# Kernel optimization log

Hardware: AMD Instinct MI355X
Metric: run time of the kernel (lower is better)

The kernel has to match this reference:

```python
import jax, jax.numpy as jnp
import numpy as np


def setup_inputs() -> dict:
    key = jax.random.key(0)
    k1, k2, k3 = jax.random.split(key, 3)
    b, n, h, d = 2, 2048, 16, 64
    q = jax.random.normal(k1, (b, n, h, d), dtype=jnp.float32)
    k = jax.random.normal(k2, (b, n, h, d), dtype=jnp.float32)
    v = jax.random.normal(k3, (b, n, h, d), dtype=jnp.float32)
    return {"q": q, "k": k, "v": v, "is_causal": 1}


def reference(q, k, v, is_causal):
    # q, k, v: [b, n, h, d] -> attention computed in [b, h, n, d] layout
    b, n, h, d = q.shape
    scale = 1.0 / jnp.sqrt(jnp.asarray(d, dtype=q.dtype))
    # scores: [b, h, n_q, n_k]
    scores = jnp.einsum("bqhd,bkhd->bhqk", q, k) * scale
    if is_causal:
        causal_mask = jnp.triu(jnp.ones((n, n), dtype=bool), k=1)  # True above diag
        scores = jnp.where(causal_mask[None, None], -jnp.inf, scores)
    attn = jax.nn.softmax(scores, axis=-1)
    out = jnp.einsum("bhqk,bkhd->bqhd", attn, v)  # back to [b, n, h, d]
    return out
```

## Files before the change

kernel.cpp:

```cpp
#include <hip/hip_runtime.h>
#include <hip/hip_bf16.h>

namespace {

constexpr int Nn = 2048;
constexpr int Hh = 16;
constexpr int Dd = 64;
constexpr int ROWSTR = Hh * Dd;
constexpr int KVB = 64;
constexpr int NTILES = Nn / KVB;
constexpr size_t IMG_TILE = 16384;
constexpr size_t WS_NEED = (size_t)32 * NTILES * IMG_TILE;

typedef __bf16 bf16x8 __attribute__((ext_vector_type(8)));
typedef __bf16 bf16x4 __attribute__((ext_vector_type(4)));
typedef float  f32x16 __attribute__((ext_vector_type(16)));

constexpr float MSHIFT = 16.0f;

__device__ __forceinline__ void gload_lds16(const char* g, char* l) {
  __builtin_amdgcn_global_load_lds(
      (const __attribute__((address_space(1))) void*)g,
      (__attribute__((address_space(3))) void*)l, 16, 0, 0);
}
__device__ __forceinline__ void drain_vmcnt0() {
  asm volatile("s_waitcnt vmcnt(0)" ::: "memory");
}

__global__ __launch_bounds__(256, 2) void prep_kernel(
    const float* __restrict__ Kg, const float* __restrict__ Vg,
    char* __restrict__ ws) {
  const int bid = blockIdx.x;
  const int bh  = bid & 31;
  const int T   = bid >> 5;
  const int tid = threadIdx.x;
  const int b = bh >> 4, h = bh & 15;
  const size_t base = ((size_t)b * Nn * Hh + h) * Dd;
  const float* kp = Kg + base;
  const float* vp = Vg + base;
  char* img = ws + (size_t)(bh * NTILES + T) * IMG_TILE;

  {
    const int row = tid >> 2;
    const int seg = tid & 3;
    const float* kr = kp + (size_t)(T * 64 + row) * ROWSTR + seg * 16;
    float4 f0 = ((const float4*)kr)[0];
    float4 f1 = ((const float4*)kr)[1];
    float4 f2 = ((const float4*)kr)[2];
    float4 f3 = ((const float4*)kr)[3];
    const int half = row >> 5, l31r = row & 31;
    char* slotp = img + (half * 4 + seg) * 1024;
    bf16x8 w0 = { (__bf16)f0.x, (__bf16)f0.y, (__bf16)f0.z, (__bf16)f0.w,
                  (__bf16)f1.x, (__bf16)f1.y, (__bf16)f1.z, (__bf16)f1.w };
    bf16x8 w1 = { (__bf16)f2.x, (__bf16)f2.y, (__bf16)f2.z, (__bf16)f2.w,
                  (__bf16)f3.x, (__bf16)f3.y, (__bf16)f3.z, (__bf16)f3.w };
    *(bf16x8*)(slotp + l31r * 16) = w0;
    *(bf16x8*)(slotp + (l31r + 32) * 16) = w1;
  }
  char* imgV = img + 8192;
#pragma unroll
  for (int e2 = 0; e2 < 2; ++e2) {
    const int e = e2 * 256 + tid;
    const int slotV = e >> 6, lane = e & 63;
    const int kc = slotV >> 1, df = slotV & 1;
    const int l31e = lane & 31, g2e = lane >> 5;
    const int d = 32 * df + l31e;
    const size_t kv0 = (size_t)(T * 64 + 16 * kc + 4 * g2e);
    const float* vb = vp + d;
    bf16x8 w;
#pragma unroll
    for (int i2 = 0; i2 < 4; ++i2) w[i2]     = (__bf16)vb[(kv0 + i2) * ROWSTR];
#pragma unroll
    for (int i2 = 0; i2 < 4; ++i2) w[4 + i2] = (__bf16)vb[(kv0 + 8 + i2) * ROWSTR];
    *(bf16x8*)(imgV + slotV * 1024 + lane * 16) = w;
  }
}

__global__ __launch_bounds__(256, 2) void fattn_kernel(
    const float* __restrict__ Qg, const char* __restrict__ ws,
    const int* __restrict__ flag, float* __restrict__ Og) {
  __shared__ __align__(16) char smem[2][2][16384];

  const int tid  = threadIdx.x;
  const int lane = tid & 63;
  const int wv   = tid >> 6;
  const int l31  = lane & 31;
  const int g2   = lane >> 5;

  const int bid  = blockIdx.x;
  const int r    = bid >> 1;
  const int side = bid & 1;
  const int bh   = ((r & 7) << 2) | ((r >> 3) & 3);
  const int j    = r >> 5;
  const int Tq   = side ? j : (15 - j);
  const int b    = bh >> 4;
  const int h    = bh & 15;
  const int causal = flag[0];

  const size_t base = ((size_t)b * Nn * Hh + h) * Dd;
  const float* qp = Qg + base;
  const char*  img = ws + (size_t)bh * NTILES * IMG_TILE;
  float*       op = Og + base;

  const float SCALE = 0.125f * 1.44269504088896340736f;

  bf16x8 vone;
#pragma unroll
  for (int e = 0; e < 8; ++e) vone[e] = (__bf16)1.0f;

  const int qs  = Tq * 128 + wv * 32;
  const int NI  = causal ? (Tq + 1) : (NTILES / 2);
  const int TLw = causal ? (2 * Tq + (wv >> 1)) : (NTILES - 1);

  bf16x8 qf[4];
#pragma unroll
  for (int dc = 0; dc < 4; ++dc) {
    const float* qrow = qp + (size_t)(qs + l31) * ROWSTR + dc * 16 + g2 * 8;
    float4 a = *(const float4*)qrow;
    float4 c = *(const float4*)(qrow + 4);
    qf[dc][0] = (__bf16)(a.x * SCALE); qf[dc][1] = (__bf16)(a.y * SCALE);
    qf[dc][2] = (__bf16)(a.z * SCALE); qf[dc][3] = (__bf16)(a.w * SCALE);
    qf[dc][4] = (__bf16)(c.x * SCALE); qf[dc][5] = (__bf16)(c.y * SCALE);
    qf[dc][6] = (__bf16)(c.z * SCALE); qf[dc][7] = (__bf16)(c.w * SCALE);
  }

  f32x16 acc0 = {};
  f32x16 acc1 = {};
  f32x16 accl = {};

#pragma unroll
  for (int it = 0; it < 8; ++it)
    gload_lds16(img + (it * 256 + tid) * 16,
                &smem[0][0][0] + (it * 256 + tid) * 16);
  __builtin_amdgcn_sched_barrier(0);

  for (int i = 0; i < NI; ++i) {
    drain_vmcnt0();
    __syncthreads();
    if (i + 1 < NI) {
      const char* src = img + (size_t)(2 * i + 2) * IMG_TILE;
      char* dst = &smem[(i + 1) & 1][0][0];
#pragma unroll
      for (int it = 0; it < 8; ++it)
        gload_lds16(src + (it * 256 + tid) * 16, dst + (it * 256 + tid) * 16);
      __builtin_amdgcn_sched_barrier(0);
    }

#pragma unroll
    for (int halfT = 0; halfT < 2; ++halfT) {
      const int tt = 2 * i + halfT;
      if (tt <= TLw) {
        const char* kb = &smem[i & 1][halfT][0];
        const char* vb = kb + 8192;

        f32x16 s0, s1;
#pragma unroll
        for (int rr = 0; rr < 16; ++rr) { s0[rr] = -MSHIFT; s1[rr] = -MSHIFT; }
        __builtin_amdgcn_s_setprio(1);
#pragma unroll
        for (int dc = 0; dc < 4; ++dc) {
          bf16x8 kf0 = *(const bf16x8*)(kb + (dc)     * 1024 + lane * 16);
          bf16x8 kf1 = *(const bf16x8*)(kb + (4 + dc) * 1024 + lane * 16);
          s0 = __builtin_amdgcn_mfma_f32_32x32x16_bf16(kf0, qf[dc], s0, 0, 0, 0);
          s1 = __builtin_amdgcn_mfma_f32_32x32x16_bf16(kf1, qf[dc], s1, 0, 0, 0);
        }
        __builtin_amdgcn_s_setprio(0);

        if (causal && tt == TLw) {
          const int kvb = tt * KVB;
          const int qrow = qs + l31;
#pragma unroll
          for (int rr = 0; rr < 16; ++rr) {
            int rm = (rr & 3) + ((rr >> 2) << 3) + (g2 << 2);
            if (kvb + rm > qrow)      s0[rr] = -INFINITY;
            if (kvb + 32 + rm > qrow) s1[rr] = -INFINITY;
          }
        }

#pragma unroll
        for (int rr = 0; rr < 16; ++rr) {
          s0[rr] = __builtin_amdgcn_exp2f(s0[rr]);
          s1[rr] = __builtin_amdgcn_exp2f(s1[rr]);
        }

        bf16x8 pa[4];
#pragma unroll
        for (int kc = 0; kc < 4; ++kc) {
          const f32x16& sv = (kc < 2) ? s0 : s1;
          const int rbase = (kc & 1) * 8;
#pragma unroll
          for (int jj = 0; jj < 8; ++jj) pa[kc][jj] = (__bf16)sv[rbase + jj];
        }

        __builtin_amdgcn_s_setprio(1);
#pragma unroll
        for (int kc = 0; kc < 4; ++kc) {
          bf16x8 vf0 = *(const bf16x8*)(vb + (kc * 2)     * 1024 + lane * 16);
          bf16x8 vf1 = *(const bf16x8*)(vb + (kc * 2 + 1) * 1024 + lane * 16);
          acc0 = __builtin_amdgcn_mfma_f32_32x32x16_bf16(pa[kc], vf0, acc0, 0, 0, 0);
          acc1 = __builtin_amdgcn_mfma_f32_32x32x16_bf16(pa[kc], vf1, acc1, 0, 0, 0);
          accl = __builtin_amdgcn_mfma_f32_32x32x16_bf16(pa[kc], vone, accl, 0, 0, 0);
        }
        __builtin_amdgcn_s_setprio(0);
      }
    }
  }

#pragma unroll
  for (int rr = 0; rr < 16; ++rr) {
    const int rm = (rr & 3) + ((rr >> 2) << 3) + (g2 << 2);
    const float li = 1.0f / accl[rr];
    const size_t row = (size_t)(qs + rm) * ROWSTR;
    op[row + l31]      = acc0[rr] * li;
    op[row + 32 + l31] = acc1[rr] * li;
  }
}

__device__ __forceinline__ int swzK(int row, int colByte) {
  return (row * 128 + colByte) ^ ((row & 7) << 4);
}
__device__ __forceinline__ int swzV(int row, int colByte) {
  return (row * 128 + colByte) ^ (((row & 7) << 4) | (((row >> 3) & 1) << 3));
}
struct SR { float4 k[4]; float v[16]; };
__device__ __forceinline__ void fb_issue(const float* kp, const float* vp,
                                         int kv0, int tid, SR& s) {
#pragma unroll
  for (int it = 0; it < 4; ++it) {
    int idx = it * 256 + tid;
    int kvr = idx >> 4, c4 = idx & 15;
    s.k[it] = *(const float4*)(kp + (size_t)(kv0 + kvr) * ROWSTR + c4 * 4);
  }
#pragma unroll
  for (int it = 0; it < 4; ++it) {
    int idx = it * 256 + tid;
    int d8 = idx & 63, kv4 = idx >> 6;
#pragma unroll
    for (int i2 = 0; i2 < 4; ++i2)
      s.v[it * 4 + i2] = vp[(size_t)(kv0 + kv4 * 4 + i2) * ROWSTR + d8];
  }
}
__device__ __forceinline__ void fb_write(char* kb, char* vb, int tid, const SR& s) {
#pragma unroll
  for (int it = 0; it < 4; ++it) {
    int idx = it * 256 + tid;
    int kvr = idx >> 4, c4 = idx & 15;
    bf16x4 w = { (__bf16)s.k[it].x, (__bf16)s.k[it].y,
                 (__bf16)s.k[it].z, (__bf16)s.k[it].w };
    *(bf16x4*)(kb + swzK(kvr, c4 * 8)) = w;
  }
#pragma unroll
  for (int it = 0; it < 4; ++it) {
    int idx = it * 256 + tid;
    int d8 = idx & 63, kv4 = idx >> 6;
    bf16x4 w = { (__bf16)s.v[it * 4 + 0], (__bf16)s.v[it * 4 + 1],
                 (__bf16)s.v[it * 4 + 2], (__bf16)s.v[it * 4 + 3] };
    *(bf16x4*)(vb + swzV(d8, kv4 * 8)) = w;
  }
}
__global__ __launch_bounds__(256, 2) void fattn_fb(
    const float* __restrict__ Qg, const float* __restrict__ Kg,
    const float* __restrict__ Vg, const int* __restrict__ flag,
    float* __restrict__ Og) {
  __shared__ char smem[16384];
  const int tid  = threadIdx.x;
  const int lane = tid & 63;
  const int wv   = tid >> 6;
  const int l31  = lane & 31;
  const int g2   = lane >> 5;
  const int bid = blockIdx.x;
  const int pidx = bid >> 1;
  const int side = bid & 1;
  const int bh  = ((pidx & 7) << 2) | (pidx >> 6);
  const int ti  = (pidx >> 3) & 7;
  const int b   = bh >> 4;
  const int h   = bh & 15;
  const int causal = flag[0];
  const int Tq  = side ? ti : (15 - ti);
  const size_t base = ((size_t)b * Nn * Hh + h) * Dd;
  const float* qp = Qg + base;
  const float* kp = Kg + base;
  const float* vp = Vg + base;
  float*       op = Og + base;
  const float SCALE = 0.125f * 1.44269504088896340736f;
  const int qs = Tq * 128 + wv * 32;
  const int Tblock = causal ? (2 * Tq + 2) : NTILES;
  const int Twave  = causal ? ((qs + 31) / KVB + 1) : NTILES;
  bf16x8 qf[4];
#pragma unroll
  for (int dc = 0; dc < 4; ++dc) {
    const float* qrow = qp + (size_t)(qs + l31) * ROWSTR + dc * 16 + g2 * 8;
    float4 a = *(const float4*)qrow;
    float4 c = *(const float4*)(qrow + 4);
    qf[dc][0] = (__bf16)(a.x * SCALE); qf[dc][1] = (__bf16)(a.y * SCALE);
    qf[dc][2] = (__bf16)(a.z * SCALE); qf[dc][3] = (__bf16)(a.w * SCALE);
    qf[dc][4] = (__bf16)(c.x * SCALE); qf[dc][5] = (__bf16)(c.y * SCALE);
    qf[dc][6] = (__bf16)(c.z * SCALE); qf[dc][7] = (__bf16)(c.w * SCALE);
  }
  f32x16 acc0 = {}, acc1 = {};
  float m_run = -INFINITY, l_run = 0.0f;
  SR st;
  fb_issue(kp, vp, 0, tid, st);
  fb_write(smem, smem + 8192, tid, st);
  for (int t = 0; t < Tblock; ++t) {
    __syncthreads();
    const bool pf = (t + 1 < Tblock);
    if (pf) fb_issue(kp, vp, (t + 1) * KVB, tid, st);
    if (t < Twave) {
      const char* kb = smem;
      const char* vb = smem + 8192;
      f32x16 s0 = {}, s1 = {};
#pragma unroll
      for (int dc = 0; dc < 4; ++dc) {
        bf16x8 kf0 = *(const bf16x8*)(kb + swzK(l31,      32 * dc + 16 * g2));
        bf16x8 kf1 = *(const bf16x8*)(kb + swzK(32 + l31, 32 * dc + 16 * g2));
        s0 = __builtin_amdgcn_mfma_f32_32x32x16_bf16(kf0, qf[dc], s0, 0, 0, 0);
        s1 = __builtin_amdgcn_mfma_f32_32x32x16_bf16(kf1, qf[dc], s1, 0, 0, 0);
      }
      if (causal && t == Twave - 1) {
        const int kvb = t * KVB;
        const int qrow = qs + l31;
#pragma unroll
        for (int rr = 0; rr < 16; ++rr) {
          int rm = (rr & 3) + ((rr >> 2) << 3) + (g2 << 2);
          if (kvb + rm > qrow)      s0[rr] = -INFINITY;
          if (kvb + 32 + rm > qrow) s1[rr] = -INFINITY;
        }
      }
      float p8[8];
#pragma unroll
      for (int e = 0; e < 8; ++e)
        p8[e] = fmaxf(fmaxf(s0[e], s0[e + 8]), fmaxf(s1[e], s1[e + 8]));
      float mt = fmaxf(fmaxf(fmaxf(p8[0], p8[1]), fmaxf(p8[2], p8[3])),
                       fmaxf(fmaxf(p8[4], p8[5]), fmaxf(p8[6], p8[7])));
      mt = fmaxf(mt, __shfl_xor(mt, 32));
      const float mnew = fmaxf(m_run, mt);
#pragma unroll
      for (int rr = 0; rr < 16; ++rr) {
        s0[rr] = __builtin_amdgcn_exp2f(s0[rr] - mnew);
        s1[rr] = __builtin_amdgcn_exp2f(s1[rr] - mnew);
      }
      float q8[8];
#pragma unroll
      for (int e = 0; e < 8; ++e)
        q8[e] = (s0[e] + s0[e + 8]) + (s1[e] + s1[e + 8]);
      float rs = ((q8[0] + q8[1]) + (q8[2] + q8[3])) +
                 ((q8[4] + q8[5]) + (q8[6] + q8[7]));
      rs += __shfl_xor(rs, 32);
      if (__all(mt <= m_run)) {
        l_run += rs;
      } else {
        const float alpha = __builtin_amdgcn_exp2f(m_run - mnew);
#pragma unroll
        for (int rr = 0; rr < 16; ++rr) {
          float at = __shfl(alpha, (rr & 3) + ((rr >> 2) << 3) + (g2 << 2));
          acc0[rr] *= at;
          acc1[rr] *= at;
        }
        l_run = l_run * alpha + rs;
        m_run = mnew;
      }
      bf16x8 pa[4];
#pragma unroll
      for (int kc = 0; kc < 4; ++kc) {
        const f32x16& sv = (kc < 2) ? s0 : s1;
        const int rbase = (kc & 1) * 8;
#pragma unroll
        for (int jj = 0; jj < 8; ++jj) pa[kc][jj] = (__bf16)sv[rbase + jj];
      }
#pragma unroll
      for (int kc = 0; kc < 4; ++kc) {
        const int cb = 32 * kc + 8 * g2;
#pragma unroll
        for (int df = 0; df < 2; ++df) {
          const int row = 32 * df + l31;
          bf16x4 v0 = *(const bf16x4*)(vb + swzV(row, cb));
          bf16x4 v1 = *(const bf16x4*)(vb + swzV(row, cb + 16));
          bf16x8 vf = __builtin_shufflevector(v0, v1, 0, 1, 2, 3, 4, 5, 6, 7);
          if (df == 0)
            acc0 = __builtin_amdgcn_mfma_f32_32x32x16_bf16(pa[kc], vf, acc0, 0, 0, 0);
          else
            acc1 = __builtin_amdgcn_mfma_f32_32x32x16_bf16(pa[kc], vf, acc1, 0, 0, 0);
        }
      }
    }
    __syncthreads();
    if (pf) fb_write(smem, smem + 8192, tid, st);
  }
  const float linv = 1.0f / l_run;
#pragma unroll
  for (int rr = 0; rr < 16; ++rr) {
    const int rm = (rr & 3) + ((rr >> 2) << 3) + (g2 << 2);
    const float li = __shfl(linv, rm);
    const size_t row = (size_t)(qs + rm) * ROWSTR;
    op[row + l31]      = acc0[rr] * li;
    op[row + 32 + l31] = acc1[rr] * li;
  }
}

}

extern "C" void kernel_launch(void* const* d_in, const int* in_sizes, int n_in,
                              void* d_out, int out_size, void* d_ws, size_t ws_size,
                              hipStream_t stream) {
  (void)in_sizes; (void)n_in; (void)out_size;
  const float* q = (const float*)d_in[0];
  const float* k = (const float*)d_in[1];
  const float* v = (const float*)d_in[2];
  const int* flag = (const int*)d_in[3];
  float* out = (float*)d_out;
  if (ws_size >= WS_NEED) {
    char* ws = (char*)d_ws;
    prep_kernel<<<dim3(1024), dim3(256), 0, stream>>>(k, v, ws);
    fattn_kernel<<<dim3(512), dim3(256), 0, stream>>>(q, ws, flag, out);
  } else {
    fattn_fb<<<dim3(512), dim3(256), 0, stream>>>(q, k, v, flag, out);
  }
}
```

Before: 46.18 us.

## Use 512-thread blocks with 256-row Q tiles, two passes, triple-buffered KV prefetch

Restructures the attention kernel into 256 blocks of 8 waves, each covering a 256-row query tile, with two passes per block that pair a long and a short causal tile for balance. KV tiles are triple-buffered in LDS with a two-ahead prefetch and a partial vmcnt wait, replacing the double buffer with a full drain. This aims to hide global-to-LDS latency and share each KV load across more waves, at the cost of 96KB of LDS per block, which may limit residency to one block per CU, and only 256 blocks launched.

```diff
diff --git a/kernel.cpp b/kernel.cpp
--- a/kernel.cpp
+++ b/kernel.cpp
@@ -22,9 +22,6 @@
   __builtin_amdgcn_global_load_lds(
       (const __attribute__((address_space(1))) void*)g,
       (__attribute__((address_space(3))) void*)l, 16, 0, 0);
-}
-__device__ __forceinline__ void drain_vmcnt0() {
-  asm volatile("s_waitcnt vmcnt(0)" ::: "memory");
 }
 
 __global__ __launch_bounds__(256, 2) void prep_kernel(
@@ -76,10 +73,10 @@
   }
 }
 
-__global__ __launch_bounds__(256, 2) void fattn_kernel(
+__global__ __launch_bounds__(512, 2) void fattn_kernel(
     const float* __restrict__ Qg, const char* __restrict__ ws,
     const int* __restrict__ flag, float* __restrict__ Og) {
-  __shared__ __align__(16) char smem[2][2][16384];
+  __shared__ __align__(16) char smem[3][32768];
 
   const int tid  = threadIdx.x;
   const int lane = tid & 63;
@@ -87,14 +84,11 @@
   const int l31  = lane & 31;
   const int g2   = lane >> 5;
 
-  const int bid  = blockIdx.x;
-  const int r    = bid >> 1;
-  const int side = bid & 1;
-  const int bh   = ((r & 7) << 2) | ((r >> 3) & 3);
-  const int j    = r >> 5;
-  const int Tq   = side ? j : (15 - j);
-  const int b    = bh >> 4;
-  const int h    = bh & 15;
+  const int bid = blockIdx.x;
+  const int bh  = ((bid & 7) << 2) | ((bid >> 3) & 3);
+  const int jp  = bid >> 5;
+  const int b   = bh >> 4;
+  const int h   = bh & 15;
   const int causal = flag[0];
 
   const size_t base = ((size_t)b * Nn * Hh + h) * Dd;
@@ -108,111 +102,129 @@
 #pragma unroll
   for (int e = 0; e < 8; ++e) vone[e] = (__bf16)1.0f;
 
-  const int qs  = Tq * 128 + wv * 32;
-  const int NI  = causal ? (Tq + 1) : (NTILES / 2);
-  const int TLw = causal ? (2 * Tq + (wv >> 1)) : (NTILES - 1);
-
-  bf16x8 qf[4];
-#pragma unroll
-  for (int dc = 0; dc < 4; ++dc) {
-    const float* qrow = qp + (size_t)(qs + l31) * ROWSTR + dc * 16 + g2 * 8;
-    float4 a = *(const float4*)qrow;
-    float4 c = *(const float4*)(qrow + 4);
-    qf[dc][0] = (__bf16)(a.x * SCALE); qf[dc][1] = (__bf16)(a.y * SCALE);
-    qf[dc][2] = (__bf16)(a.z * SCALE); qf[dc][3] = (__bf16)(a.w * SCALE);
-    qf[dc][4] = (__bf16)(c.x * SCALE); qf[dc][5] = (__bf16)(c.y * SCALE);
-    qf[dc][6] = (__bf16)(c.z * SCALE); qf[dc][7] = (__bf16)(c.w * SCALE);
-  }
-
-  f32x16 acc0 = {};
-  f32x16 acc1 = {};
-  f32x16 accl = {};
-
-#pragma unroll
-  for (int it = 0; it < 8; ++it)
-    gload_lds16(img + (it * 256 + tid) * 16,
-                &smem[0][0][0] + (it * 256 + tid) * 16);
-  __builtin_amdgcn_sched_barrier(0);
-
-  for (int i = 0; i < NI; ++i) {
-    drain_vmcnt0();
+  for (int pass = 0; pass < 2; ++pass) {
+    const int T256 = pass ? jp : (7 - jp);
+    const int qs   = T256 * 256 + wv * 32;
+    const int NI   = causal ? (2 * T256 + 2) : (NTILES / 2);
+    const int TLw  = causal ? (4 * T256 + (wv >> 1)) : (NTILES - 1);
+
     __syncthreads();
-    if (i + 1 < NI) {
-      const char* src = img + (size_t)(2 * i + 2) * IMG_TILE;
-      char* dst = &smem[(i + 1) & 1][0][0];
-#pragma unroll
-      for (int it = 0; it < 8; ++it)
-        gload_lds16(src + (it * 256 + tid) * 16, dst + (it * 256 + tid) * 16);
+
+    bf16x8 qf[4];
+#pragma unroll
+    for (int dc = 0; dc < 4; ++dc) {
+      const float* qrow = qp + (size_t)(qs + l31) * ROWSTR + dc * 16 + g2 * 8;
+      float4 a = *(const float4*)qrow;
+      float4 c = *(const float4*)(qrow + 4);
+      qf[dc][0] = (__bf16)(a.x * SCALE); qf[dc][1] = (__bf16)(a.y * SCALE);
+      qf[dc][2] = (__bf16)(a.z * SCALE); qf[dc][3] = (__bf16)(a.w * SCALE);
+      qf[dc][4] = (__bf16)(c.x * SCALE); qf[dc][5] = (__bf16)(c.y * SCALE);
+      qf[dc][6] = (__bf16)(c.z * SCALE); qf[dc][7] = (__bf16)(c.w * SCALE);
+    }
+
+    f32x16 acc0 = {};
+    f32x16 acc1 = {};
+    f32x16 accl = {};
+
+#pragma unroll
+    for (int it = 0; it < 4; ++it)
+      gload_lds16(img + (it * 512 + tid) * 16,
+                  &smem[0][0] + (it * 512 + tid) * 16);
+    if (NI > 1) {
+#pragma unroll
+      for (int it = 0; it < 4; ++it)
+        gload_lds16(img + 2 * IMG_TILE + (it * 512 + tid) * 16,
+                    &smem[1][0] + (it * 512 + tid) * 16);
+    }
+    __builtin_amdgcn_sched_barrier(0);
+
+    for (int i = 0; i < NI; ++i) {
+      if (i + 1 < NI) {
+        asm volatile("s_waitcnt vmcnt(4)" ::: "memory");
+      } else {
+        asm volatile("s_waitcnt vmcnt(0)" ::: "memory");
+      }
       __builtin_amdgcn_sched_barrier(0);
+      __syncthreads();
+
+      if (i + 2 < NI) {
+        const char* src = img + (size_t)(2 * i + 4) * IMG_TILE;
+        char* dst = &smem[(i + 2) % 3][0];
+#pragma unroll
+        for (int it = 0; it < 4; ++it)
+          gload_lds16(src + (it * 512 + tid) * 16, dst + (it * 512 + tid) * 16);
+        __builtin_amdgcn_sched_barrier(0);
+      }
+
+      const char* pb = &smem[i % 3][0];
+#pragma unroll
+      for (int halfT = 0; halfT < 2; ++halfT) {
+        const int tt = 2 * i + halfT;
+        if (tt <= TLw) {
+          const char* kb = pb + halfT * 16384;
+          const char* vb = kb + 8192;
+
+          f32x16 s0, s1;
+#pragma unroll
+          for (int rr = 0; rr < 16; ++rr) { s0[rr] = -MSHIFT; s1[rr] = -MSHIFT; }
+          __builtin_amdgcn_s_setprio(1);
+#pragma unroll
+          for (int dc = 0; dc < 4; ++dc) {
+            bf16x8 kf0 = *(const bf16x8*)(kb + (dc)     * 1024 + lane * 16);
+            bf16x8 kf1 = *(const bf16x8*)(kb + (4 + dc) * 1024 + lane * 16);
+            s0 = __builtin_amdgcn_mfma_f32_32x32x16_bf16(kf0, qf[dc], s0, 0, 0, 0);
+            s1 = __builtin_amdgcn_mfma_f32_32x32x16_bf16(kf1, qf[dc], s1, 0, 0, 0);
+          }
+          __builtin_amdgcn_s_setprio(0);
+
+          if (causal && tt == TLw) {
+            const int kvb = tt * KVB;
+            const int qrow = qs + l31;
+#pragma unroll
+            for (int rr = 0; rr < 16; ++rr) {
+              int rm = (rr & 3) + ((rr >> 2) << 3) + (g2 << 2);
+              if (kvb + rm > qrow)      s0[rr] = -INFINITY;
+              if (kvb + 32 + rm > qrow) s1[rr] = -INFINITY;
+            }
+          }
+
+#pragma unroll
+          for (int rr = 0; rr < 16; ++rr) {
+            s0[rr] = __builtin_amdgcn_exp2f(s0[rr]);
+            s1[rr] = __builtin_amdgcn_exp2f(s1[rr]);
+          }
+
+          bf16x8 pa[4];
+#pragma unroll
+          for (int kc = 0; kc < 4; ++kc) {
+            const f32x16& sv = (kc < 2) ? s0 : s1;
+            const int rbase = (kc & 1) * 8;
+#pragma unroll
+            for (int jj = 0; jj < 8; ++jj) pa[kc][jj] = (__bf16)sv[rbase + jj];
+          }
+
+          __builtin_amdgcn_s_setprio(1);
+#pragma unroll
+          for (int kc = 0; kc < 4; ++kc) {
+            bf16x8 vf0 = *(const bf16x8*)(vb + (kc * 2)     * 1024 + lane * 16);
+            bf16x8 vf1 = *(const bf16x8*)(vb + (kc * 2 + 1) * 1024 + lane * 16);
+            acc0 = __builtin_amdgcn_mfma_f32_32x32x16_bf16(pa[kc], vf0, acc0, 0, 0, 0);
+            acc1 = __builtin_amdgcn_mfma_f32_32x32x16_bf16(pa[kc], vf1, acc1, 0, 0, 0);
+            accl = __builtin_amdgcn_mfma_f32_32x32x16_bf16(pa[kc], vone, accl, 0, 0, 0);
+          }
+          __builtin_amdgcn_s_setprio(0);
+        }
+      }
     }
 
 #pragma unroll
-    for (int halfT = 0; halfT < 2; ++halfT) {
-      const int tt = 2 * i + halfT;
-      if (tt <= TLw) {
-        const char* kb = &smem[i & 1][halfT][0];
-        const char* vb = kb + 8192;
-
-        f32x16 s0, s1;
-#pragma unroll
-        for (int rr = 0; rr < 16; ++rr) { s0[rr] = -MSHIFT; s1[rr] = -MSHIFT; }
-        __builtin_amdgcn_s_setprio(1);
-#pragma unroll
-        for (int dc = 0; dc < 4; ++dc) {
-          bf16x8 kf0 = *(const bf16x8*)(kb + (dc)     * 1024 + lane * 16);
-          bf16x8 kf1 = *(const bf16x8*)(kb + (4 + dc) * 1024 + lane * 16);
-          s0 = __builtin_amdgcn_mfma_f32_32x32x16_bf16(kf0, qf[dc], s0, 0, 0, 0);
-          s1 = __builtin_amdgcn_mfma_f32_32x32x16_bf16(kf1, qf[dc], s1, 0, 0, 0);
-        }
-        __builtin_amdgcn_s_setprio(0);
-
-        if (causal && tt == TLw) {
-          const int kvb = tt * KVB;
-          const int qrow = qs + l31;
-#pragma unroll
-          for (int rr = 0; rr < 16; ++rr) {
-            int rm = (rr & 3) + ((rr >> 2) << 3) + (g2 << 2);
-            if (kvb + rm > qrow)      s0[rr] = -INFINITY;
-            if (kvb + 32 + rm > qrow) s1[rr] = -INFINITY;
-          }
-        }
-
-#pragma unroll
-        for (int rr = 0; rr < 16; ++rr) {
-          s0[rr] = __builtin_amdgcn_exp2f(s0[rr]);
-          s1[rr] = __builtin_amdgcn_exp2f(s1[rr]);
-        }
-
-        bf16x8 pa[4];
-#pragma unroll
-        for (int kc = 0; kc < 4; ++kc) {
-          const f32x16& sv = (kc < 2) ? s0 : s1;
-          const int rbase = (kc & 1) * 8;
-#pragma unroll
-          for (int jj = 0; jj < 8; ++jj) pa[kc][jj] = (__bf16)sv[rbase + jj];
-        }
-
-        __builtin_amdgcn_s_setprio(1);
-#pragma unroll
-        for (int kc = 0; kc < 4; ++kc) {
-          bf16x8 vf0 = *(const bf16x8*)(vb + (kc * 2)     * 1024 + lane * 16);
-          bf16x8 vf1 = *(const bf16x8*)(vb + (kc * 2 + 1) * 1024 + lane * 16);
-          acc0 = __builtin_amdgcn_mfma_f32_32x32x16_bf16(pa[kc], vf0, acc0, 0, 0, 0);
-          acc1 = __builtin_amdgcn_mfma_f32_32x32x16_bf16(pa[kc], vf1, acc1, 0, 0, 0);
-          accl = __builtin_amdgcn_mfma_f32_32x32x16_bf16(pa[kc], vone, accl, 0, 0, 0);
-        }
-        __builtin_amdgcn_s_setprio(0);
-      }
+    for (int rr = 0; rr < 16; ++rr) {
+      const int rm = (rr & 3) + ((rr >> 2) << 3) + (g2 << 2);
+      const float li = 1.0f / accl[rr];
+      const size_t row = (size_t)(qs + rm) * ROWSTR;
+      op[row + l31]      = acc0[rr] * li;
+      op[row + 32 + l31] = acc1[rr] * li;
     }
-  }
-
-#pragma unroll
-  for (int rr = 0; rr < 16; ++rr) {
-    const int rm = (rr & 3) + ((rr >> 2) << 3) + (g2 << 2);
-    const float li = 1.0f / accl[rr];
-    const size_t row = (size_t)(qs + rm) * ROWSTR;
-    op[row + l31]      = acc0[rr] * li;
-    op[row + 32 + l31] = acc1[rr] * li;
   }
 }
 
@@ -412,7 +424,7 @@
   if (ws_size >= WS_NEED) {
     char* ws = (char*)d_ws;
     prep_kernel<<<dim3(1024), dim3(256), 0, stream>>>(k, v, ws);
-    fattn_kernel<<<dim3(512), dim3(256), 0, stream>>>(q, ws, flag, out);
+    fattn_kernel<<<dim3(256), dim3(512), 0, stream>>>(q, ws, flag, out);
   } else {
     fattn_fb<<<dim3(512), dim3(256), 0, stream>>>(q, k, v, flag, out);
   }
```

Result: slower. 60.72 us (+31.5%).
